# Kernel optimization log

Hardware: AMD Instinct MI355X
Metric: run time of the kernel (lower is better)

## Reference

```python
import jax, jax.numpy as jnp
import numpy as np

B, T, N, C = 4, 6, 512, 8
HID, FEAT, EMB, IN_DIM = 64, 16, 32, 1
KS, KC, HORIZON = 3, 2, 3
ALPHA = 3.0

def _init(key, shape):
    fin = shape[-2] if len(shape) >= 2 else shape[-1]
    return jax.random.normal(key, shape, dtype=jnp.float32) * (1.0 / fin) ** 0.5

def setup_inputs():
    ks = jax.random.split(jax.random.key(0), 32)
    L_enc = (IN_DIM + FEAT + HID) * KS * KC
    L_dec = (HID + FEAT + HID) * KS * KC
    return {
        "X_seq": jax.random.normal(ks[0], (B, T, N, C), dtype=jnp.float32),
        "As": jax.random.uniform(ks[1], (N, N), dtype=jnp.float32) / N,
        "Ac": jax.random.uniform(ks[2], (C, C), dtype=jnp.float32) / C,
        "feature": jax.random.normal(ks[3], (N, FEAT), dtype=jnp.float32),
        "Wu_S": _init(ks[4], (C, HID)), "Wv_S": _init(ks[5], (C, HID)),
        "Wu_C": _init(ks[6], (N, HID)), "Wv_C": _init(ks[7], (N, HID)),
        "mfS_w1": _init(ks[8], (4, 2, 256)), "mfS_b1": jnp.zeros((4, 256), jnp.float32),
        "mfS_w2": _init(ks[9], (4, 256, 256)), "mfS_b2": jnp.zeros((4, 256), jnp.float32),
        "mfC_w1": _init(ks[10], (4, 2, 256)), "mfC_b1": jnp.zeros((4, 256), jnp.float32),
        "mfC_w2": _init(ks[11], (4, 256, 256)), "mfC_b2": jnp.zeros((4, 256), jnp.float32),
        "enc_gW": _init(ks[12], (L_enc, 2 * HID)), "enc_gb": jnp.zeros((2 * HID,), jnp.float32),
        "enc_cW": _init(ks[13], (L_enc, HID)), "enc_cb": jnp.zeros((HID,), jnp.float32),
        "dec_gW": _init(ks[14], (L_dec, 2 * HID)), "dec_gb": jnp.zeros((2 * HID,), jnp.float32),
        "dec_cW": _init(ks[15], (L_dec, HID)), "dec_cb": jnp.zeros((HID,), jnp.float32),
        "out_w1": _init(ks[16], (HID, EMB)), "out_b1": jnp.zeros((EMB,), jnp.float32),
        "out_w2": _init(ks[17], (EMB, IN_DIM)), "out_b2": jnp.zeros((IN_DIM,), jnp.float32),
    }

def _mlp(x, w1, b1, w2, b2):
    return jax.nn.relu(x @ w1 + b1) @ w2 + b2

def _mixed_fusion(A, P, w1, b1, w2, b2):
    # node_feat = [rowsum(A), rowsum(P)]; key/value MLPs indexed 0:key_A 1:key_P 2:val_A 3:val_P
    nf = jnp.stack([A.sum(-1), P.sum(-1)], axis=-1)            # [n, 2]
    An, Pn = A @ nf, P @ nf
    key = _mlp(An, w1[0], b1[0], w2[0], b2[0]) + _mlp(Pn, w1[1], b1[1], w2[1], b2[1])
    val = _mlp(An, w1[2], b1[2], w2[2], b2[2]) + _mlp(Pn, w1[3], b1[3], w2[3], b2[3])
    a = jax.nn.sigmoid(key @ val.T)
    return a * A + (1.0 - a) * P

def _adaptive_graph(Xf, Wu, Wv):
    U = jnp.tanh(ALPHA * Xf @ Wu)                              # [b,t,n,h]
    V = jnp.tanh(ALPHA * Xf @ Wv)
    M = jnp.einsum('btnh,btmh->nm', U, V)
    # Ps = softmax(relu(M - M^T)) matches einsum pair in torch source
    return jax.nn.softmax(jax.nn.relu(M - M.T), axis=-1)

def _cheby(G, K):
    mats = [jnp.eye(G.shape[0], dtype=G.dtype), G]
    for _ in range(2, K):
        mats.append(2.0 * G @ mats[-1] - mats[-2])
    return jnp.stack(mats[:K], axis=0)                         # [K, n, n]

def _bdg(X, Gs_set, Gc_set, W, b):
    # X: [b,n,c,l]; fused Ks x Kc Chebyshev mode products; cat order (k, j, l) matches torch cat
    t1 = jnp.einsum('bncl,knm->kbmcl', X, Gs_set)
    t2 = jnp.einsum('kbmcl,jcd->bmdkjl', t1, Gc_set)
    feat = t2.reshape(t2.shape[0], t2.shape[1], t2.shape[2], -1)
    return feat @ W + b

def _cell(Xt, Ht, featx, Gs_set, Gc_set, gW, gb, cW, cb):
    XH = jnp.concatenate([Xt, Ht, featx], axis=-1)
    uv = _bdg(XH, Gs_set, Gc_set, gW, gb)
    update = jax.nn.sigmoid(uv[..., :HID])
    reset = jax.nn.sigmoid(uv[..., HID:])
    cand_in = jnp.concatenate([Xt, reset * Ht, featx], axis=-1)
    cand = jnp.tanh(_bdg(cand_in, Gs_set, Gc_set, cW, cb))
    return (1.0 - update) * Ht + update * cand

def _forward(X_seq, As, Ac, feature, Wu_S, Wv_S, Wu_C, Wv_C,
             mfS_w1, mfS_b1, mfS_w2, mfS_b2, mfC_w1, mfC_b1, mfC_w2, mfC_b2,
             enc_gW, enc_gb, enc_cW, enc_cb, dec_gW, dec_gb, dec_cW, dec_cb,
             out_w1, out_b1, out_w2, out_b2):
    # MGP_Gen: adaptive spatial / categorical graphs fused with priors
    Ps = _adaptive_graph(X_seq, Wu_S, Wv_S)
    Gs = _mixed_fusion(As, Ps, mfS_w1, mfS_b1, mfS_w2, mfS_b2)
    Xc = jnp.swapaxes(X_seq, 2, 3)                             # [b,t,c,n]
    Pc = _adaptive_graph(Xc, Wu_C, Wv_C)
    Gc = _mixed_fusion(Ac, Pc, mfC_w1, mfC_b1, mfC_w2, mfC_b2)
    Gs_set, Gc_set = _cheby(Gs, KS), _cheby(Gc, KC)
    featx = jnp.broadcast_to(feature[None, :, None, :], (B, N, C, FEAT))
    X5 = X_seq[..., None]                                      # [b,t,n,c,1]
    Ht = jnp.zeros((B, N, C, HID), dtype=X_seq.dtype)
    for t in range(T):                                         # encoder GRU over history
        Ht = _cell(X5[:, t], Ht, featx, Gs_set, Gc_set, enc_gW, enc_gb, enc_cW, enc_cb)
    deco_in, Hd = Ht, Ht
    outs = []
    for _ in range(HORIZON):
        Hd = _cell(deco_in, Hd, featx, Gs_set, Gc_set, dec_gW, dec_gb, dec_cW, dec_cb)
        outs.append(_mlp(Hd, out_w1, out_b1, out_w2, out_b2))
        deco_in = Hd
    return jnp.stack(outs, axis=1)                             # [b, horizon, n, c, 1]

def reference(X_seq, As, Ac, feature, Wu_S, Wv_S, Wu_C, Wv_C, mfS_w1, mfS_b1, mfS_w2, mfS_b2, mfC_w1, mfC_b1, mfC_w2, mfC_b2, enc_gW, enc_gb, enc_cW, enc_cb, dec_gW, dec_gb, dec_cW, dec_cb, out_w1, out_b1, out_w2, out_b2):
    return _forward(X_seq, As, Ac, feature, Wu_S, Wv_S, Wu_C, Wv_C, mfS_w1, mfS_b1, mfS_w2, mfS_b2, mfC_w1, mfC_b1, mfC_w2, mfC_b2, enc_gW, enc_gb, enc_cW, enc_cb, dec_gW, dec_gb, dec_cW, dec_cb, out_w1, out_b1, out_w2, out_b2)
```

## Files before the change

### kernel.cpp

```cpp
#include <hip/hip_runtime.h>
#include <math.h>

constexpr int kB = 4, kT = 6, kN = 512, kC = 8;
constexpr int kH = 64, kF = 16, kE = 32;
constexpr int kKS = 3, kKC = 2, kHOR = 3;
constexpr int kBT = kB * kT;
constexpr int kRK = kBT * kH;
constexpr int L_ENC = 1 + kH + kF;
constexpr int L_DEC = kH + kH + kF;
constexpr int PL_ENC = 96;
constexpr int PL_DEC = 160;
constexpr int KP_ENC = 3 * PL_ENC;
constexpr int KP_DEC = 3 * PL_DEC;
constexpr float kALPHA = 3.0f;

typedef unsigned short ushortT;
typedef short short8 __attribute__((ext_vector_type(8)));
typedef float f32x4 __attribute__((ext_vector_type(4)));

__device__ __forceinline__ float sigm(float x) { return 1.0f / (1.0f + __expf(-x)); }

__device__ __forceinline__ ushortT f2bf(float f) {
    union { float f; unsigned int u; } v; v.f = f;
    unsigned int r = v.u + 0x7fffu + ((v.u >> 16) & 1u);
    return (ushortT)(r >> 16);
}

__device__ __forceinline__ void fma44(const float4& a, const float4& b, float acc[4][4]) {
    acc[0][0] += a.x*b.x; acc[0][1] += a.x*b.y; acc[0][2] += a.x*b.z; acc[0][3] += a.x*b.w;
    acc[1][0] += a.y*b.x; acc[1][1] += a.y*b.y; acc[1][2] += a.y*b.z; acc[1][3] += a.y*b.w;
    acc[2][0] += a.z*b.x; acc[2][1] += a.z*b.y; acc[2][2] += a.z*b.z; acc[2][3] += a.z*b.w;
    acc[3][0] += a.w*b.x; acc[3][1] += a.w*b.y; acc[3][2] += a.w*b.z; acc[3][3] += a.w*b.w;
}


__global__ __launch_bounds__(256) void k_uvproj_s(
    const float* __restrict__ X, const float* __restrict__ Wu, const float* __restrict__ Wv,
    float* __restrict__ Upr, float* __restrict__ Vpr)
{
    int idx = blockIdx.x * blockDim.x + threadIdx.x;
    if (idx >= kN * kBT * kH) return;
    int h = idx % kH; int bt = (idx / kH) % kBT; int n = idx / (kH * kBT);
    const float* xr = X + ((size_t)bt * kN + n) * kC;
    float u = 0.f, v = 0.f;
#pragma unroll
    for (int c = 0; c < kC; ++c) { float x = xr[c]; u += x * Wu[c*kH + h]; v += x * Wv[c*kH + h]; }
    Upr[(size_t)n * kRK + bt * kH + h] = tanhf(kALPHA * u);
    Vpr[(size_t)n * kRK + bt * kH + h] = tanhf(kALPHA * v);
}

__global__ __launch_bounds__(512) void k_uvproj_c2(
    const float* __restrict__ X, const float* __restrict__ WuC, const float* __restrict__ WvC,
    float* __restrict__ Uc, float* __restrict__ Vc)
{
    __shared__ float Xs[4096];
    __shared__ float Wus[4096], Wvs[4096];
    int bt = blockIdx.x, tid = threadIdx.x;
    for (int i = tid; i < 4096; i += 512) Xs[i] = X[(size_t)bt*4096 + i];
    int c = tid >> 6, h = tid & 63;
    float u = 0.f, v = 0.f;
    for (int n0 = 0; n0 < 512; n0 += 64) {
        __syncthreads();
        for (int i = tid; i < 4096; i += 512) { Wus[i] = WuC[n0*64 + i]; Wvs[i] = WvC[n0*64 + i]; }
        __syncthreads();
#pragma unroll 8
        for (int nn = 0; nn < 64; ++nn) {
            float x = Xs[(n0+nn)*8 + c];
            u += x * Wus[nn*64 + h];
            v += x * Wvs[nn*64 + h];
        }
    }
    Uc[(size_t)bt*512 + c*64 + h] = tanhf(kALPHA * u);
    Vc[(size_t)bt*512 + c*64 + h] = tanhf(kALPHA * v);
}

__global__ __launch_bounds__(512) void k_mc2(
    const float* __restrict__ Uc, const float* __restrict__ Vc, float* __restrict__ Mc)
{
    __shared__ float red[512];
    int tid = threadIdx.x;
    int cd = tid & 63, kc = tid >> 6;
    int c = cd >> 3, d = cd & 7;
    float s = 0.f;
    for (int q = kc*192; q < kc*192 + 192; ++q) {
        int bt = q >> 6, h = q & 63;
        s += Uc[(size_t)bt*512 + c*64 + h] * Vc[(size_t)bt*512 + d*64 + h];
    }
    red[tid] = s; __syncthreads();
    for (int st = 256; st >= 64; st >>= 1) { if (tid < st) red[tid] += red[tid + st]; __syncthreads(); }
    if (tid < 64) Mc[tid] = red[tid];
}

__global__ __launch_bounds__(256) void k_nfa(const float* __restrict__ A, float* __restrict__ nf)
{
    int i = blockIdx.x, tid = threadIdx.x;
// ... 147 lines not shown
        rsA[i] = a;
    }
    __syncthreads();
    if (tid < 16) {
        int i = tid >> 1, comp = tid & 1;
        float an = 0.f, pn = 0.f;
#pragma unroll
        for (int j = 0; j < 8; ++j) {
            float nfj = comp ? 1.f : rsA[j];
            an += Ac[i*8+j] * nfj; pn += Pcs[i*8+j] * nfj;
        }
        Ans[i*2+comp] = an; Pns[i*2+comp] = pn;
    }
    __syncthreads();
    for (int e = tid; e < 2048; e += 256) {
        int i = e >> 8, o = e & 255;
        hA[i][o] = fmaxf(Ans[i*2]*w1[qa*512 + o] + Ans[i*2+1]*w1[qa*512 + 256 + o] + b1[qa*256 + o], 0.f);
        hP[i][o] = fmaxf(Pns[i*2]*w1[qp*512 + o] + Pns[i*2+1]*w1[qp*512 + 256 + o] + b1[qp*256 + o], 0.f);
    }
    __syncthreads();
    for (int e = tid; e < 512; e += 256) {
        int i = e >> 6, oc = c0 + (e & 63);
        float s = b2[qa*256 + oc] + b2[qp*256 + oc];
        for (int k = 0; k < 256; ++k)
            s += hA[i][k]*w2[(size_t)qa*65536 + k*256 + oc] + hP[i][k]*w2[(size_t)qp*65536 + k*256 + oc];
        keyval[(size_t)kv*2048 + i*256 + oc] = s;
    }
}

__global__ void k_gcfuse2(const float* __restrict__ keyval, const float* __restrict__ Mc,
                          const float* __restrict__ Ac, float* __restrict__ GcF)
{
    __shared__ float Pcs[64];
    int t = threadIdx.x; if (t >= 64) return;
    if (t < 8) {
        int i = t;
        float row[8]; float mx = -1e30f;
#pragma unroll
        for (int j = 0; j < 8; ++j) { float v = fmaxf(Mc[i*8+j] - Mc[j*8+i], 0.f); row[j] = v; mx = fmaxf(mx, v); }
        float s = 0.f;
#pragma unroll
        for (int j = 0; j < 8; ++j) { row[j] = __expf(row[j] - mx); s += row[j]; }
        float inv = 1.f / s;
#pragma unroll
        for (int j = 0; j < 8; ++j) Pcs[i*8+j] = row[j] * inv;
    }
    __syncthreads();
    int c = t >> 3, d = t & 7;
    const float* key = keyval;
    const float* val = keyval + 2048;
    float s = 0.f;
    for (int k = 0; k < 256; ++k) s += key[c*256 + k] * val[d*256 + k];
    float a = sigm(s);
    GcF[c*8 + d] = a*Ac[c*8 + d] + (1.f - a)*Pcs[c*8 + d];
}


__global__ void k_transp(const float* __restrict__ G, ushortT* __restrict__ Gt)
{
    __shared__ float tile[32][33];
    int bx = blockIdx.x * 32, by = blockIdx.y * 32;
    int x = threadIdx.x, y0 = threadIdx.y;
    for (int yy = y0; yy < 32; yy += 8) tile[yy][x] = G[(size_t)(by+yy)*kN + bx + x];
    __syncthreads();
    for (int yy = y0; yy < 32; yy += 8) Gt[(size_t)(bx+yy)*kN + by + x] = f2bf(tile[x][yy]);
}

__global__ __launch_bounds__(256) void k_prep_wt(
    const float* __restrict__ W, ushortT* __restrict__ WT,
    int L, int PL, int KP, int outW, int mode)
{
    int idx = blockIdx.x * blockDim.x + threadIdx.x;
    if (idx >= 2 * outW * KP) return;
    int qp = idx % KP, o = idx / KP;
    int kk = qp / PL, l = qp - kk * PL;
    int lo;
    if (mode == 1) lo = (l < 64) ? l + 1 : (l == 64) ? 0 : (l < 80) ? L : (l - 15);
    else lo = l;
    int j = o / outW, oo = o - j * outW;
    float v = (lo < L) ? W[(size_t)((kk*2 + j)*L + lo) * outW + oo] : 0.f;
    WT[idx] = f2bf(v);
}

__global__ __launch_bounds__(256) void k_cheby_mfma(
    const ushortT* __restrict__ Gst, ushortT* __restrict__ Gst2)
{
    __shared__ short sA[128][40];
    __shared__ short sB[128][40];
    int tid = threadIdx.x;
    int m0 = blockIdx.y * 128, j0 = blockIdx.x * 128;
    int w = tid >> 6, lane = tid & 63, wr = w >> 1, wc = w & 1;
    f32x4 acc[4][4];
#pragma unroll
    for (int i = 0; i < 4; ++i)
#pragma unroll
        for (int j = 0; j < 4; ++j) acc[i][j] = (f32x4){0.f, 0.f, 0.f, 0.f};
    for (int k0 = 0; k0 < kN; k0 += 32) {
        {
            int row = tid >> 1, lc = (tid & 1) * 16;
            const ushortT* p = Gst + (size_t)(m0 + row)*kN + k0 + lc;
            *(short8*)&sA[row][lc]     = *(const short8*)p;
            *(short8*)&sA[row][lc + 8] = *(const short8*)(p + 8);
        }
        {
            int kr = tid & 31, jc = (tid >> 5) * 8;
#pragma unroll
            for (int rep = 0; rep < 2; ++rep) {
                short8 v = *(const short8*)(Gst + (size_t)(k0 + kr)*kN + j0 + jc + rep*64);
#pragma unroll
                for (int i = 0; i < 8; ++i) sB[jc + rep*64 + i][kr] = v[i];
            }
        }
        __syncthreads();
        short8 af[4], bfr[4];
#pragma unroll
        for (int mi = 0; mi < 4; ++mi)
            af[mi] = *(const short8*)&sA[wr*64 + mi*16 + (lane & 15)][(lane >> 4) * 8];
#pragma unroll
        for (int ni = 0; ni < 4; ++ni)
            bfr[ni] = *(const short8*)&sB[wc*64 + ni*16 + (lane & 15)][(lane >> 4) * 8];
#pragma unroll
        for (int mi = 0; mi < 4; ++mi)
#pragma unroll
            for (int ni = 0; ni < 4; ++ni)
                acc[mi][ni] = __builtin_amdgcn_mfma_f32_16x16x32_bf16(af[mi], bfr[ni], acc[mi][ni], 0, 0, 0);
        __syncthreads();
    }
#pragma unroll
    for (int mi = 0; mi < 4; ++mi) {
#pragma unroll
        for (int ni = 0; ni < 4; ++ni) {
            int row0 = m0 + wr*64 + mi*16 + (lane >> 4) * 4;
            int col  = j0 + wc*64 + ni*16 + (lane & 15);
#pragma unroll
            for (int q = 0; q < 4; ++q) {
                int row = row0 + q;
                Gst2[(size_t)row*kN + col] = f2bf(2.f*acc[mi][ni][q] - (row == col ? 1.f : 0.f));
            }
        }
    }
}

template<int CLP, int PL, int ACTW, int OFF>
__global__ __launch_bounds__(256) void k_t1m(
    const ushortT* __restrict__ Gst, const ushortT* __restrict__ Xin, ushortT* __restrict__ Yout)
{
    __shared__ short sA[128][40];
    __shared__ short sB[128][40];
    int tid = threadIdx.x;
    int ki = blockIdx.z >> 2, b = blockIdx.z & 3;
    const ushortT* A = Gst + (size_t)ki * kN * kN;
    const ushortT* B = Xin + (size_t)b * kN * CLP;
    ushortT* C = Yout + (size_t)(ki*4 + b) * kN * CLP;
    int m0 = blockIdx.y * 128, j0 = blockIdx.x * 128;
    int w = tid >> 6, lane = tid & 63, wr = w >> 1, wc = w & 1;
    f32x4 acc[4][4];
#pragma unroll
    for (int i = 0; i < 4; ++i)
#pragma unroll
        for (int j = 0; j < 4; ++j) acc[i][j] = (f32x4){0.f, 0.f, 0.f, 0.f};

    for (int k0 = 0; k0 < kN; k0 += 32) {
        {
            int row = tid >> 1, lc = (tid & 1) * 16;
            const ushortT* p = A + (size_t)(m0 + row)*kN + k0 + lc;
            *(short8*)&sA[row][lc]     = *(const short8*)p;
            *(short8*)&sA[row][lc + 8] = *(const short8*)(p + 8);
        }
        {
            int kr = tid & 31, jc = (tid >> 5) * 8;
#pragma unroll
            for (int rep = 0; rep < 2; ++rep) {
                int j = j0 + jc + rep*64;
                int cg = j / ACTW;
                int col = cg*PL + OFF + (j - cg*ACTW);
                short8 v = *(const short8*)(B + (size_t)(k0 + kr)*CLP + col);
#pragma unroll
                for (int i = 0; i < 8; ++i) sB[jc + rep*64 + i][kr] = v[i];
            }
        }
        __syncthreads();
        short8 af[4], bfr[4];
#pragma unroll
        for (int mi = 0; mi < 4; ++mi)
            af[mi] = *(const short8*)&sA[wr*64 + mi*16 + (lane & 15)][(lane >> 4) * 8];
#pragma unroll
        for (int ni = 0; ni < 4; ++ni)
            bfr[ni] = *(const short8*)&sB[wc*64 + ni*16 + (lane & 15)][(lane >> 4) * 8];
#pragma unroll
        for (int mi = 0; mi < 4; ++mi)
#pragma unroll
            for (int ni = 0; ni < 4; ++ni)
                acc[mi][ni] = __builtin_amdgcn_mfma_f32_16x16x32_bf16(af[mi], bfr[ni], acc[mi][ni], 0, 0, 0);
        __syncthreads();
    }
#pragma unroll
    for (int mi = 0; mi < 4; ++mi) {
#pragma unroll
        for (int ni = 0; ni < 4; ++ni) {
            int row = m0 + wr*64 + mi*16 + (lane >> 4) * 4;
            int fj = j0 + wc*64 + ni*16;
            int cg = fj / ACTW;
            int col = cg*PL + OFF + (fj - cg*ACTW) + (lane & 15);
#pragma unroll
            for (int q = 0; q < 4; ++q)
                C[(size_t)(row + q)*CLP + col] = f2bf(acc[mi][ni][q]);
        }
    }
}

template<int PL, int KP, int XOFF>
__global__ __launch_bounds__(256) void k_gates_f(
    ushortT* __restrict__ XH, const ushortT* __restrict__ Yb,
    const ushortT* __restrict__ WT, const float* __restrict__ GcM,
    const float* __restrict__ gb, const float* __restrict__ Ht,
    float* __restrict__ upd)
{
    __shared__ short sA[64][40];
    __shared__ short sB[256][40];
    __shared__ float sEp[32][260];
    __shared__ float GcS[64], gbS[128];
    int tid = threadIdx.x;
    int r0 = blockIdx.x * 64;
    int b = r0 >> 12, rr = r0 & 4095;
    const ushortT* src0 = XH + (size_t)r0 * PL;
    const ushortT* src1 = Yb + ((size_t)b * 4096 + rr) * PL;
    const ushortT* src2 = Yb + ((size_t)(4 + b) * 4096 + rr) * PL;
    if (tid < 64) GcS[tid] = GcM[tid];
    if (tid >= 64 && tid < 192) gbS[tid - 64] = gb[tid - 64];
    int w = tid >> 6, lane = tid & 63;
    f32x4 acc[4][4];
#pragma unroll
    for (int i = 0; i < 4; ++i)
#pragma unroll
        for (int j = 0; j < 4; ++j) acc[i][j] = (f32x4){0.f, 0.f, 0.f, 0.f};

    for (int k0 = 0; k0 < KP; k0 += 32) {
        int kk = k0 / PL, l0 = k0 - kk * PL;
        const ushortT* Ap = (kk == 0) ? src0 : (kk == 1) ? src1 : src2;
        {
            int row = tid >> 2, lc = (tid & 3) * 8;
            *(short8*)&sA[row][lc] = *(const short8*)(Ap + (size_t)row*PL + l0 + lc);
        }
        {
            const ushortT* p = WT + (size_t)tid*KP + k0;
            *(short8*)&sB[tid][0]  = *(const short8*)(p);
            *(short8*)&sB[tid][8]  = *(const short8*)(p + 8);
            *(short8*)&sB[tid][16] = *(const short8*)(p + 16);
            *(short8*)&sB[tid][24] = *(const short8*)(p + 24);
        }
        __syncthreads();
        short8 af[4], bfr[4];
#pragma unroll
        for (int mi = 0; mi < 4; ++mi)
            af[mi] = *(const short8*)&sA[mi*16 + (lane & 15)][(lane >> 4) * 8];
#pragma unroll
        for (int ni = 0; ni < 4; ++ni)
            bfr[ni] = *(const short8*)&sB[w*64 + ni*16 + (lane & 15)][(lane >> 4) * 8];
#pragma unroll
        for (int mi = 0; mi < 4; ++mi)
#pragma unroll
            for (int ni = 0; ni < 4; ++ni)
                acc[mi][ni] = __builtin_amdgcn_mfma_f32_16x16x32_bf16(af[mi], bfr[ni], acc[mi][ni], 0, 0, 0);
        __syncthreads();
    }
    for (int chunk = 0; chunk < 2; ++chunk) {
#pragma unroll
        for (int mi2 = 0; mi2 < 2; ++mi2) {
            int mi = chunk*2 + mi2;
#pragma unroll
            for (int ni = 0; ni < 4; ++ni)
#pragma unroll
                for (int q = 0; q < 4; ++q)
                    sEp[mi2*16 + (lane >> 4)*4 + q][w*64 + ni*16 + (lane & 15)] = acc[mi][ni][q];
        }
        __syncthreads();
        for (int it = 0; it < 16; ++it) {
            int idx = it*256 + tid;
            int o = idx & 127, rloc = idx >> 7;
            int r = r0 + chunk*32 + rloc;
            int d = r & 7, bb = rloc & ~7;
            float pre = sEp[rloc][o] + gbS[o];
#pragma unroll
            for (int c = 0; c < 8; ++c) pre += GcS[c*8 + d] * sEp[bb + c][128 + o];
            float g = sigm(pre);
            if (o < 64) upd[(size_t)r*64 + o] = g;
            else {
                int h = o - 64;
                XH[(size_t)r*PL + XOFF + h] = f2bf(g * Ht[(size_t)r*64 + h]);
            }
        }
        __syncthreads();
    }
}

template<int PL, int KP>
__global__ __launch_bounds__(256) void k_cand_f(
    const ushortT* __restrict__ XH, const ushortT* __restrict__ Yb,
    const ushortT* __restrict__ WT, const float* __restrict__ GcM,
    const float* __restrict__ cb, const float* __restrict__ upd,
    float* __restrict__ Ht)
{
    __shared__ short sA[64][40];
    __shared__ short sB[128][40];
    __shared__ float sEp[64][132];
    __shared__ float GcS[64], cbS[64];
    int tid = threadIdx.x;
    int r0 = blockIdx.x * 64;
    int b = r0 >> 12, rr = r0 & 4095;
    const ushortT* src0 = XH + (size_t)r0 * PL;
    const ushortT* src1 = Yb + ((size_t)b * 4096 + rr) * PL;
    const ushortT* src2 = Yb + ((size_t)(4 + b) * 4096 + rr) * PL;
    if (tid < 64) GcS[tid] = GcM[tid];
    if (tid >= 64 && tid < 128) cbS[tid - 64] = cb[tid - 64];
    int w = tid >> 6, lane = tid & 63;
    f32x4 acc[4][2];
#pragma unroll
    for (int i = 0; i < 4; ++i)
#pragma unroll
        for (int j = 0; j < 2; ++j) acc[i][j] = (f32x4){0.f, 0.f, 0.f, 0.f};

    for (int k0 = 0; k0 < KP; k0 += 32) {
        int kk = k0 / PL, l0 = k0 - kk * PL;
        const ushortT* Ap = (kk == 0) ? src0 : (kk == 1) ? src1 : src2;
        {
            int row = tid >> 2, lc = (tid & 3) * 8;
            *(short8*)&sA[row][lc] = *(const short8*)(Ap + (size_t)row*PL + l0 + lc);
        }
        {
            int col = tid >> 1, seg = (tid & 1) * 16;
            const ushortT* p = WT + (size_t)col*KP + k0 + seg;
            *(short8*)&sB[col][seg]     = *(const short8*)p;
            *(short8*)&sB[col][seg + 8] = *(const short8*)(p + 8);
        }
        __syncthreads();
        short8 af[4], bfr[2];
#pragma unroll
        for (int mi = 0; mi < 4; ++mi)
            af[mi] = *(const short8*)&sA[mi*16 + (lane & 15)][(lane >> 4) * 8];
#pragma unroll
        for (int ni = 0; ni < 2; ++ni)
            bfr[ni] = *(const short8*)&sB[w*32 + ni*16 + (lane & 15)][(lane >> 4) * 8];
#pragma unroll
        for (int mi = 0; mi < 4; ++mi)
#pragma unroll
            for (int ni = 0; ni < 2; ++ni)
                acc[mi][ni] = __builtin_amdgcn_mfma_f32_16x16x32_bf16(af[mi], bfr[ni], acc[mi][ni], 0, 0, 0);
        __syncthreads();
    }
#pragma unroll
    for (int mi = 0; mi < 4; ++mi)
#pragma unroll
        for (int ni = 0; ni < 2; ++ni)
#pragma unroll
            for (int q = 0; q < 4; ++q)
                sEp[mi*16 + (lane >> 4)*4 + q][w*32 + ni*16 + (lane & 15)] = acc[mi][ni][q];
    __syncthreads();
    for (int it = 0; it < 16; ++it) {
        int idx = it*256 + tid;
        int o = idx & 63, rloc = idx >> 6;
        int r = r0 + rloc;
        int d = r & 7, bb = rloc & ~7;
        float pre = sEp[rloc][o] + cbS[o];
#pragma unroll
        for (int c = 0; c < 8; ++c) pre += GcS[c*8 + d] * sEp[bb + c][64 + o];
        float cv = tanhf(pre);
        float u = upd[(size_t)r*64 + o];
        float h0 = Ht[(size_t)r*64 + o];
        Ht[(size_t)r*64 + o] = (1.f - u)*h0 + u*cv;
    }
}


__global__ __launch_bounds__(256) void k_build_enc(
    const float* __restrict__ X, int t, const float* __restrict__ Ht,
    const float* __restrict__ featr, ushortT* __restrict__ XH)
{
    int idx = blockIdx.x * blockDim.x + threadIdx.x;
    if (idx >= 16384 * PL_ENC) return;
    int l = idx % PL_ENC; int r = idx / PL_ENC;
    int c = r & 7; int m = (r >> 3) & 511; int b = r >> 12;
    float v;
    if (l < 64)            v = Ht[(size_t)r*kH + l];
    else if (l == 64)      v = X[(((size_t)b*kT + t)*kN + m)*kC + c];
    else if (l < 80)       v = 0.f;
    else                   v = featr[m*kF + (l - 80)];
    XH[idx] = f2bf(v);
}

__global__ __launch_bounds__(256) void k_build_dec(
    const float* __restrict__ Ht, const float* __restrict__ featr, ushortT* __restrict__ XH)
{
    int idx = blockIdx.x * blockDim.x + threadIdx.x;
    if (idx >= 16384 * PL_DEC) return;
    int l = idx % PL_DEC; int r = idx / PL_DEC;
    int m = (r >> 3) & 511;
    float v;
    if (l < kH)            v = Ht[(size_t)r*kH + l];
    else if (l < 2*kH)     v = Ht[(size_t)r*kH + l - kH];
    else if (l < L_DEC)    v = featr[m*kF + l - 2*kH];
    else                   v = 0.f;
    XH[idx] = f2bf(v);
}

__global__ __launch_bounds__(256) void k_outmlp(
    const float* __restrict__ Hd, const float* __restrict__ w1, const float* __restrict__ b1,
    const float* __restrict__ w2, const float* __restrict__ b2, float* __restrict__ out, int hz)
{
    int idx = blockIdx.x * blockDim.x + threadIdx.x;
    if (idx >= kB*kN*kC) return;
    int c = idx % kC; int m = (idx / kC) % kN; int b = idx / (kC*kN);
    const float* h = Hd + (size_t)idx * kH;
    float hreg[kH];
#pragma unroll
    for (int k = 0; k < kH; ++k) hreg[k] = h[k];
    float acc = b2[0];
    for (int e = 0; e < kE; ++e) {
        float s = b1[e];
#pragma unroll
        for (int k = 0; k < kH; ++k) s += hreg[k] * w1[k*kE + e];
        acc += fmaxf(s, 0.f) * w2[e];
    }
    out[((size_t)(b*kHOR + hz)*kN + m)*kC + c] = acc;
}

extern "C" void kernel_launch(void* const* d_in, const int* in_sizes, int n_in,
                              void* d_out, int out_size, void* d_ws, size_t ws_size,
                              hipStream_t stream)
{
    (void)in_sizes; (void)n_in; (void)out_size; (void)ws_size;
    const float* X      = (const float*)d_in[0];
    const float* As     = (const float*)d_in[1];
    const float* Ac     = (const float*)d_in[2];
    const float* featr  = (const float*)d_in[3];
    const float* WuS    = (const float*)d_in[4];
    const float* WvS    = (const float*)d_in[5];
    const float* WuC    = (const float*)d_in[6];
    const float* WvC    = (const float*)d_in[7];
    const float* mfS_w1 = (const float*)d_in[8];
    const float* mfS_b1 = (const float*)d_in[9];
    const float* mfS_w2 = (const float*)d_in[10];
    const float* mfS_b2 = (const float*)d_in[11];
    const float* mfC_w1 = (const float*)d_in[12];
    const float* mfC_b1 = (const float*)d_in[13];
    const float* mfC_w2 = (const float*)d_in[14];
    const float* mfC_b2 = (const float*)d_in[15];
    const float* enc_gW = (const float*)d_in[16];
    const float* enc_gb = (const float*)d_in[17];
    const float* enc_cW = (const float*)d_in[18];
    const float* enc_cb = (const float*)d_in[19];
    const float* dec_gW = (const float*)d_in[20];
    const float* dec_gb = (const float*)d_in[21];
    const float* dec_cW = (const float*)d_in[22];
    const float* dec_cb = (const float*)d_in[23];
    const float* out_w1 = (const float*)d_in[24];
    const float* out_b1 = (const float*)d_in[25];
    const float* out_w2 = (const float*)d_in[26];
    const float* out_b2 = (const float*)d_in[27];
    float* out = (float*)d_out;
    float* ws = (float*)d_ws;

    float* Ht     = ws;
    float* updb   = Ht + 1048576;
    float* Gg     = updb + 1048576;
    float* Gs     = Gg + 4194304;
    float* smallf = Gs + 262144;
    float* nfS = smallf;
    float* AnS = nfS + 1024;
    float* PnS = AnS + 1024;
    float* McB = PnS + 1024;
    float* GcF = McB + 64;
    float* kvC = GcF + 64;
    ushortT* XHb  = (ushortT*)(smallf + 8192);
    ushortT* Yb   = XHb + 2621440;
    ushortT* GstB = Yb + 5242880;
    ushortT* WTg_e = GstB + 524288;
    ushortT* WTc_e = WTg_e + 73728;
    ushortT* WTg_d = WTc_e + 36864;
    ushortT* WTc_d = WTg_d + 122880;
    float* Upr   = Gg;
    float* Vpr   = Upr + 786432;
    float* part  = Vpr + 786432;
    float* Ms    = part + 1048576;
    float* Ps    = Ms + 262144;
    float* hidAP = Ps + 262144;
    float* keyS  = hidAP + 262144;
    float* valS  = keyS + 131072;
    float* w2tK  = valS + 131072;
    float* w2tV  = w2tK + 131072;
    float* Uc    = w2tV + 131072;
    float* Vc    = Uc + 12288;

    constexpr int CLP_ENC = kC * PL_ENC;
    constexpr int CLP_DEC = kC * PL_DEC;

    hipMemsetAsync(Ht, 0, (size_t)16384 * kH * sizeof(float), stream);

    k_prep_wt<<<(2*128*KP_ENC + 255)/256, 256, 0, stream>>>(enc_gW, WTg_e, L_ENC, PL_ENC, KP_ENC, 128, 1);
    k_prep_wt<<<(2*64 *KP_ENC + 255)/256, 256, 0, stream>>>(enc_cW, WTc_e, L_ENC, PL_ENC, KP_ENC, 64, 1);
    k_prep_wt<<<(2*128*KP_DEC + 255)/256, 256, 0, stream>>>(dec_gW, WTg_d, L_DEC, PL_DEC, KP_DEC, 128, 0);
    k_prep_wt<<<(2*64 *KP_DEC + 255)/256, 256, 0, stream>>>(dec_cW, WTc_d, L_DEC, PL_DEC, KP_DEC, 64, 0);
    k_prep_w2t<<<512, 256, 0, stream>>>(mfS_w2, w2tK, w2tV);

    k_uvproj_s<<<(kN*kBT*kH + 255)/256, 256, 0, stream>>>(X, WuS, WvS, Upr, Vpr);
    k_gemm_ntsk<<<dim3(8, 8, 4), 256, 0, stream>>>(Upr, Vpr, part, 512, 512, 1536, 384);
    k_redep<<<1024, 256, 0, stream>>>(part, 4, 262144, 512, Ms, 0, nullptr, nullptr);
    k_nfa<<<kN, 256, 0, stream>>>(As, nfS);
    k_softmax_anpn<<<kN, 256, 0, stream>>>(Ms, As, nfS, Ps, AnS, PnS);
    k_mlp1cat<<<1024, 256, 0, stream>>>(AnS, PnS, mfS_w1, mfS_b1, 0, 1, hidAP);
    k_gemm_ntsk<<<dim3(4, 8, 2), 256, 0, stream>>>(hidAP, w2tK, part, 512, 256, 512, 256);
    k_redep<<<512, 256, 0, stream>>>(part, 2, 131072, 256, keyS, 2, mfS_b2, mfS_b2 + 256);
    k_mlp1cat<<<1024, 256, 0, stream>>>(AnS, PnS, mfS_w1, mfS_b1, 2, 3, hidAP);
    k_gemm_ntsk<<<dim3(4, 8, 2), 256, 0, stream>>>(hidAP, w2tV, part, 512, 256, 512, 256);
    k_redep<<<512, 256, 0, stream>>>(part, 2, 131072, 256, valS, 2, mfS_b2 + 512, mfS_b2 + 768);
    k_gemm_ntsk<<<dim3(8, 8, 2), 256, 0, stream>>>(keyS, valS, part, 512, 512, 256, 128);
    k_redep<<<1024, 256, 0, stream>>>(part, 2, 262144, 512, Gs, 1, As, Ps);
    k_transp<<<dim3(16, 16), dim3(32, 8), 0, stream>>>(Gs, GstB);
    k_cheby_mfma<<<dim3(4, 4), 256, 0, stream>>>(GstB, GstB + 262144);

    k_uvproj_c2<<<kBT, 512, 0, stream>>>(X, WuC, WvC, Uc, Vc);
    k_mc2<<<1, 512, 0, stream>>>(Uc, Vc, McB);
    k_catmlp2<<<dim3(2, 4), 256, 0, stream>>>(McB, Ac, mfC_w1, mfC_b1, mfC_w2, mfC_b2, kvC);
    k_gcfuse2<<<1, 64, 0, stream>>>(kvC, McB, Ac, GcF);

    bool featDone = false;
    for (int t = 0; t < kT; ++t) {
        k_build_enc<<<(16384*PL_ENC + 255)/256, 256, 0, stream>>>(X, t, Ht, featr, XHb);
        if (!featDone) {
            k_t1m<CLP_ENC, PL_ENC, 16, 80><<<dim3(1, 4, 8), 256, 0, stream>>>(GstB, XHb, Yb);
            featDone = true;
        }
        k_t1m<CLP_ENC, PL_ENC, 80, 0><<<dim3(5, 4, 8), 256, 0, stream>>>(GstB, XHb, Yb);
        k_gates_f<PL_ENC, KP_ENC, 0><<<256, 256, 0, stream>>>(XHb, Yb, WTg_e, GcF, enc_gb, Ht, updb);
        k_t1m<CLP_ENC, PL_ENC, 64, 0><<<dim3(4, 4, 8), 256, 0, stream>>>(GstB, XHb, Yb);
        k_cand_f<PL_ENC, KP_ENC><<<256, 256, 0, stream>>>(XHb, Yb, WTc_e, GcF, enc_cb, updb, Ht);
    }

    featDone = false;
    for (int hz = 0; hz < kHOR; ++hz) {
        k_build_dec<<<(16384*PL_DEC + 255)/256, 256, 0, stream>>>(Ht, featr, XHb);
        if (!featDone) {
            k_t1m<CLP_DEC, PL_DEC, 16, 128><<<dim3(1, 4, 8), 256, 0, stream>>>(GstB, XHb, Yb);
            featDone = true;
        }
        k_t1m<CLP_DEC, PL_DEC, 128, 0><<<dim3(8, 4, 8), 256, 0, stream>>>(GstB, XHb, Yb);
        k_gates_f<PL_DEC, KP_DEC, 64><<<256, 256, 0, stream>>>(XHb, Yb, WTg_d, GcF, dec_gb, Ht, updb);
        k_t1m<CLP_DEC, PL_DEC, 64, 64><<<dim3(4, 4, 8), 256, 0, stream>>>(GstB, XHb, Yb);
        k_cand_f<PL_DEC, KP_DEC><<<256, 256, 0, stream>>>(XHb, Yb, WTc_d, GcF, dec_cb, updb, Ht);
        k_outmlp<<<(kB*kN*kC + 255)/256, 256, 0, stream>>>(Ht, out_w1, out_b1, out_w2, out_b2, out, hz);
    }
}
```

Measured before the change: 1.078 ms.

## Split gate GEMMs from epilogues, fold decoder duplicate input weights, fuse state builds

Each fused gate and candidate kernel becomes two kernels. The first is a 128-row MFMA GEMM that writes fp32 pre-activations to a scratch buffer, and the second is a per-node epilogue that applies the Gc channel mix and the nonlinearity. The decoder gate weights for the duplicated hidden input are pre-summed so K shrinks from 480 to 288, and its graph propagation only handles 64 columns instead of 128. The per-step build_enc/build_dec kernels are removed by having the candidate epilogue write the next bf16 input row, including the next X value. The output MLP is fused into the decoder epilogue. In exchange, fp32 intermediates make an extra round-trip through global memory.

```diff
diff --git a/kernel.cpp b/kernel.cpp
--- a/kernel.cpp
+++ b/kernel.cpp
@@ -11,6 +11,7 @@
 constexpr int PL_ENC = 96;
 constexpr int PL_DEC = 160;
 constexpr int KP_ENC = 3 * PL_ENC;
+constexpr int KP_DGF = 288;
 constexpr int KP_DEC = 3 * PL_DEC;
 constexpr float kALPHA = 3.0f;
 
@@ -324,6 +325,22 @@
     WT[idx] = f2bf(v);
 }
 
+__global__ __launch_bounds__(256) void k_prep_wtgd(
+    const float* __restrict__ W, ushortT* __restrict__ WT)
+{
+    int idx = blockIdx.x * blockDim.x + threadIdx.x;
+    if (idx >= 256 * KP_DGF) return;
+    int qp = idx % KP_DGF, o = idx / KP_DGF;
+    int k = qp / 96, p = qp - k * 96;
+    int j = o >> 7, oo = o & 127;
+    int base = (k*2 + j) * L_DEC;
+    float v;
+    if (p < 64)      v = W[(size_t)(base + p)*128 + oo] + W[(size_t)(base + 64 + p)*128 + oo];
+    else if (p < 80) v = W[(size_t)(base + 128 + (p - 64))*128 + oo];
+    else             v = 0.f;
+    WT[idx] = f2bf(v);
+}
+
 __global__ __launch_bounds__(256) void k_cheby_mfma(
     const ushortT* __restrict__ Gst, ushortT* __restrict__ Gst2)
 {
@@ -396,6 +413,10 @@
     ushortT* C = Yout + (size_t)(ki*4 + b) * kN * CLP;
     int m0 = blockIdx.y * 128, j0 = blockIdx.x * 128;
     int w = tid >> 6, lane = tid & 63, wr = w >> 1, wc = w & 1;
+    int kr = tid & 31, jc = (tid >> 5) * 8;
+    int colr0, colr1;
+    { int j = j0 + jc;      int cg = j / ACTW; colr0 = cg*PL + OFF + (j - cg*ACTW); }
+    { int j = j0 + jc + 64; int cg = j / ACTW; colr1 = cg*PL + OFF + (j - cg*ACTW); }
     f32x4 acc[4][4];
 #pragma unroll
     for (int i = 0; i < 4; ++i)
@@ -410,16 +431,12 @@
             *(short8*)&sA[row][lc + 8] = *(const short8*)(p + 8);
         }
         {
-            int kr = tid & 31, jc = (tid >> 5) * 8;
-#pragma unroll
-            for (int rep = 0; rep < 2; ++rep) {
-                int j = j0 + jc + rep*64;
-                int cg = j / ACTW;
-                int col = cg*PL + OFF + (j - cg*ACTW);
-                short8 v = *(const short8*)(B + (size_t)(k0 + kr)*CLP + col);
-#pragma unroll
-                for (int i = 0; i < 8; ++i) sB[jc + rep*64 + i][kr] = v[i];
-            }
+            short8 v0 = *(const short8*)(B + (size_t)(k0 + kr)*CLP + colr0);
+            short8 v1 = *(const short8*)(B + (size_t)(k0 + kr)*CLP + colr1);
+#pragma unroll
+            for (int i = 0; i < 8; ++i) sB[jc + i][kr] = v0[i];
+#pragma unroll
+            for (int i = 0; i < 8; ++i) sB[jc + 64 + i][kr] = v1[i];
         }
         __syncthreads();
         short8 af[4], bfr[4];
@@ -451,219 +468,193 @@
     }
 }
 
-template<int PL, int KP, int XOFF>
-__global__ __launch_bounds__(256) void k_gates_f(
-    ushortT* __restrict__ XH, const ushortT* __restrict__ Yb,
-    const ushortT* __restrict__ WT, const float* __restrict__ GcM,
-    const float* __restrict__ gb, const float* __restrict__ Ht,
-    float* __restrict__ upd)
-{
-    __shared__ short sA[64][40];
-    __shared__ short sB[256][40];
-    __shared__ float sEp[32][260];
-    __shared__ float GcS[64], gbS[128];
+template<int PL, int NQ, int MODE, int FN>
+__global__ __launch_bounds__(256) void k_gg(
+    const ushortT* __restrict__ XH, const ushortT* __restrict__ Yb,
+    const ushortT* __restrict__ WT, float* __restrict__ Cout)
+{
+    constexpr int BN = 32 * FN;
+    constexpr int KP = NQ * 32;
+    constexpr int Ntot = 64 * FN;
+    __shared__ short sA[128][40];
+    __shared__ short sB[BN][40];
     int tid = threadIdx.x;
-    int r0 = blockIdx.x * 64;
+    int r0 = blockIdx.y * 128, j0 = blockIdx.x * BN;
     int b = r0 >> 12, rr = r0 & 4095;
     const ushortT* src0 = XH + (size_t)r0 * PL;
-    const ushortT* src1 = Yb + ((size_t)b * 4096 + rr) * PL;
+    const ushortT* src1 = Yb + ((size_t)b       * 4096 + rr) * PL;
     const ushortT* src2 = Yb + ((size_t)(4 + b) * 4096 + rr) * PL;
-    if (tid < 64) GcS[tid] = GcM[tid];
-    if (tid >= 64 && tid < 192) gbS[tid - 64] = gb[tid - 64];
-    int w = tid >> 6, lane = tid & 63;
-    f32x4 acc[4][4];
+    int w = tid >> 6, lane = tid & 63, wr = w >> 1, wc = w & 1;
+    f32x4 acc[4][FN];
 #pragma unroll
     for (int i = 0; i < 4; ++i)
 #pragma unroll
-        for (int j = 0; j < 4; ++j) acc[i][j] = (f32x4){0.f, 0.f, 0.f, 0.f};
-
-    for (int k0 = 0; k0 < KP; k0 += 32) {
-        int kk = k0 / PL, l0 = k0 - kk * PL;
-        const ushortT* Ap = (kk == 0) ? src0 : (kk == 1) ? src1 : src2;
+        for (int j = 0; j < FN; ++j) acc[i][j] = (f32x4){0.f, 0.f, 0.f, 0.f};
+
+    for (int q = 0; q < NQ; ++q) {
+        int k, off;
+        if (MODE == 0)      { k = q/3; off = (q - k*3)*32; }
+        else if (MODE == 1) { k = q/3; int part = q - k*3; off = (part < 2) ? part*32 : 128; }
+        else                { k = q/5; off = (q - k*5)*32; }
+        const ushortT* Ap = (k == 0) ? src0 : (k == 1) ? src1 : src2;
         {
-            int row = tid >> 2, lc = (tid & 3) * 8;
-            *(short8*)&sA[row][lc] = *(const short8*)(Ap + (size_t)row*PL + l0 + lc);
-        }
-        {
-            const ushortT* p = WT + (size_t)tid*KP + k0;
-            *(short8*)&sB[tid][0]  = *(const short8*)(p);
-            *(short8*)&sB[tid][8]  = *(const short8*)(p + 8);
-            *(short8*)&sB[tid][16] = *(const short8*)(p + 16);
-            *(short8*)&sB[tid][24] = *(const short8*)(p + 24);
-        }
-        __syncthreads();
-        short8 af[4], bfr[4];
-#pragma unroll
-        for (int mi = 0; mi < 4; ++mi)
-            af[mi] = *(const short8*)&sA[mi*16 + (lane & 15)][(lane >> 4) * 8];
-#pragma unroll
-        for (int ni = 0; ni < 4; ++ni)
-            bfr[ni] = *(const short8*)&sB[w*64 + ni*16 + (lane & 15)][(lane >> 4) * 8];
-#pragma unroll
-        for (int mi = 0; mi < 4; ++mi)
-#pragma unroll
-            for (int ni = 0; ni < 4; ++ni)
-                acc[mi][ni] = __builtin_amdgcn_mfma_f32_16x16x32_bf16(af[mi], bfr[ni], acc[mi][ni], 0, 0, 0);
-        __syncthreads();
-    }
-    for (int chunk = 0; chunk < 2; ++chunk) {
-#pragma unroll
-        for (int mi2 = 0; mi2 < 2; ++mi2) {
-            int mi = chunk*2 + mi2;
-#pragma unroll
-            for (int ni = 0; ni < 4; ++ni)
-#pragma unroll
-                for (int q = 0; q < 4; ++q)
-                    sEp[mi2*16 + (lane >> 4)*4 + q][w*64 + ni*16 + (lane & 15)] = acc[mi][ni][q];
-        }
-        __syncthreads();
-        for (int it = 0; it < 16; ++it) {
-            int idx = it*256 + tid;
-            int o = idx & 127, rloc = idx >> 7;
-            int r = r0 + chunk*32 + rloc;
-            int d = r & 7, bb = rloc & ~7;
-            float pre = sEp[rloc][o] + gbS[o];
-#pragma unroll
-            for (int c = 0; c < 8; ++c) pre += GcS[c*8 + d] * sEp[bb + c][128 + o];
-            float g = sigm(pre);
-            if (o < 64) upd[(size_t)r*64 + o] = g;
-            else {
-                int h = o - 64;
-                XH[(size_t)r*PL + XOFF + h] = f2bf(g * Ht[(size_t)r*64 + h]);
-            }
-        }
-        __syncthreads();
-    }
-}
-
-template<int PL, int KP>
-__global__ __launch_bounds__(256) void k_cand_f(
-    const ushortT* __restrict__ XH, const ushortT* __restrict__ Yb,
-    const ushortT* __restrict__ WT, const float* __restrict__ GcM,
-    const float* __restrict__ cb, const float* __restrict__ upd,
-    float* __restrict__ Ht)
-{
-    __shared__ short sA[64][40];
-    __shared__ short sB[128][40];
-    __shared__ float sEp[64][132];
-    __shared__ float GcS[64], cbS[64];
-    int tid = threadIdx.x;
-    int r0 = blockIdx.x * 64;
-    int b = r0 >> 12, rr = r0 & 4095;
-    const ushortT* src0 = XH + (size_t)r0 * PL;
-    const ushortT* src1 = Yb + ((size_t)b * 4096 + rr) * PL;
-    const ushortT* src2 = Yb + ((size_t)(4 + b) * 4096 + rr) * PL;
-    if (tid < 64) GcS[tid] = GcM[tid];
-    if (tid >= 64 && tid < 128) cbS[tid - 64] = cb[tid - 64];
-    int w = tid >> 6, lane = tid & 63;
-    f32x4 acc[4][2];
-#pragma unroll
-    for (int i = 0; i < 4; ++i)
-#pragma unroll
-        for (int j = 0; j < 2; ++j) acc[i][j] = (f32x4){0.f, 0.f, 0.f, 0.f};
-
-    for (int k0 = 0; k0 < KP; k0 += 32) {
-        int kk = k0 / PL, l0 = k0 - kk * PL;
-        const ushortT* Ap = (kk == 0) ? src0 : (kk == 1) ? src1 : src2;
-        {
-            int row = tid >> 2, lc = (tid & 3) * 8;
-            *(short8*)&sA[row][lc] = *(const short8*)(Ap + (size_t)row*PL + l0 + lc);
-        }
-        {
+            int row = tid >> 1, lc = (tid & 1) * 16;
+            const ushortT* p = Ap + (size_t)row * PL + off + lc;
+            *(short8*)&sA[row][lc]     = *(const short8*)p;
+            *(short8*)&sA[row][lc + 8] = *(const short8*)(p + 8);
+        }
+        if (FN == 4) {
             int col = tid >> 1, seg = (tid & 1) * 16;
-            const ushortT* p = WT + (size_t)col*KP + k0 + seg;
+            const ushortT* p = WT + (size_t)(j0 + col)*KP + q*32 + seg;
             *(short8*)&sB[col][seg]     = *(const short8*)p;
             *(short8*)&sB[col][seg + 8] = *(const short8*)(p + 8);
-        }
-        __syncthreads();
-        short8 af[4], bfr[2];
+        } else {
+            int col = tid >> 2, seg = (tid & 3) * 8;
+            *(short8*)&sB[col][seg] = *(const short8*)(WT + (size_t)(j0 + col)*KP + q*32 + seg);
+        }
+        __syncthreads();
+        short8 af[4], bfr[FN];
 #pragma unroll
         for (int mi = 0; mi < 4; ++mi)
-            af[mi] = *(const short8*)&sA[mi*16 + (lane & 15)][(lane >> 4) * 8];
-#pragma unroll
-        for (int ni = 0; ni < 2; ++ni)
-            bfr[ni] = *(const short8*)&sB[w*32 + ni*16 + (lane & 15)][(lane >> 4) * 8];
+            af[mi] = *(const short8*)&sA[wr*64 + mi*16 + (lane & 15)][(lane >> 4) * 8];
+#pragma unroll
+        for (int ni = 0; ni < FN; ++ni)
+            bfr[ni] = *(const short8*)&sB[wc*16*FN + ni*16 + (lane & 15)][(lane >> 4) * 8];
 #pragma unroll
         for (int mi = 0; mi < 4; ++mi)
 #pragma unroll
-            for (int ni = 0; ni < 2; ++ni)
+            for (int ni = 0; ni < FN; ++ni)
                 acc[mi][ni] = __builtin_amdgcn_mfma_f32_16x16x32_bf16(af[mi], bfr[ni], acc[mi][ni], 0, 0, 0);
         __syncthreads();
     }
 #pragma unroll
-    for (int mi = 0; mi < 4; ++mi)
-#pragma unroll
-        for (int ni = 0; ni < 2; ++ni)
+    for (int mi = 0; mi < 4; ++mi) {
+#pragma unroll
+        for (int ni = 0; ni < FN; ++ni) {
+            int row = r0 + wr*64 + mi*16 + (lane >> 4) * 4;
+            int col = j0 + wc*16*FN + ni*16 + (lane & 15);
 #pragma unroll
             for (int q = 0; q < 4; ++q)
-                sEp[mi*16 + (lane >> 4)*4 + q][w*32 + ni*16 + (lane & 15)] = acc[mi][ni][q];
+                Cout[(size_t)(row + q)*Ntot + col] = acc[mi][ni][q];
+        }
+    }
+}
+
+
+template<int PL, int XOFF>
+__global__ __launch_bounds__(256) void k_gates_ep(
+    const float* __restrict__ Gg, const float* __restrict__ GcM,
+    const float* __restrict__ gb, const float* __restrict__ Ht,
+    float* __restrict__ upd, ushortT* __restrict__ XH)
+{
+    __shared__ float sG[8][256];
+    __shared__ float GcS[64];
+    int tid = threadIdx.x, bm = blockIdx.x;
+    const float* src = Gg + (size_t)bm * 2048;
+    for (int i = tid; i < 2048; i += 256) sG[i >> 8][i & 255] = src[i];
+    if (tid < 64) GcS[tid] = GcM[tid];
     __syncthreads();
-    for (int it = 0; it < 16; ++it) {
-        int idx = it*256 + tid;
-        int o = idx & 63, rloc = idx >> 6;
-        int r = r0 + rloc;
-        int d = r & 7, bb = rloc & ~7;
-        float pre = sEp[rloc][o] + cbS[o];
-#pragma unroll
-        for (int c = 0; c < 8; ++c) pre += GcS[c*8 + d] * sEp[bb + c][64 + o];
+    int d = tid >> 5, o0 = (tid & 31) * 4;
+    size_t rb = (size_t)bm * 8 + d;
+#pragma unroll
+    for (int q = 0; q < 4; ++q) {
+        int o = o0 + q;
+        float pre = sG[d][o] + gb[o];
+#pragma unroll
+        for (int c = 0; c < 8; ++c) pre += GcS[c*8 + d] * sG[c][128 + o];
+        float g = sigm(pre);
+        if (o < kH) upd[rb*kH + o] = g;
+        else {
+            int h = o - kH;
+            XH[rb*PL + XOFF + h] = f2bf(g * Ht[rb*kH + h]);
+        }
+    }
+}
+
+template<int MODE>
+__global__ __launch_bounds__(256) void k_cand_ep(
+    const float* __restrict__ Gc2, const float* __restrict__ GcM,
+    const float* __restrict__ cb, const float* __restrict__ upd,
+    float* __restrict__ Ht, ushortT* __restrict__ XHo,
+    const float* __restrict__ X, int tnext,
+    const float* __restrict__ ow1, const float* __restrict__ ob1,
+    const float* __restrict__ ow2, const float* __restrict__ ob2,
+    float* __restrict__ out, int hz)
+{
+    __shared__ float sG[8][128];
+    __shared__ float GcS[64];
+    __shared__ float Hn[8][65];
+    __shared__ float Pp[8][32];
+    int tid = threadIdx.x, bm = blockIdx.x;
+    const float* src = Gc2 + (size_t)bm * 1024;
+    for (int i = tid; i < 1024; i += 256) sG[i >> 7][i & 127] = src[i];
+    if (tid < 64) GcS[tid] = GcM[tid];
+    __syncthreads();
+    int d = tid >> 5, o0 = (tid & 31) * 2;
+    size_t rb = (size_t)bm * 8 + d;
+#pragma unroll
+    for (int jj = 0; jj < 2; ++jj) {
+        int o = o0 + jj;
+        float pre = sG[d][o] + cb[o];
+#pragma unroll
+        for (int c = 0; c < 8; ++c) pre += GcS[c*8 + d] * sG[c][64 + o];
         float cv = tanhf(pre);
-        float u = upd[(size_t)r*64 + o];
-        float h0 = Ht[(size_t)r*64 + o];
-        Ht[(size_t)r*64 + o] = (1.f - u)*h0 + u*cv;
-    }
-}
-
-
-__global__ __launch_bounds__(256) void k_build_enc(
-    const float* __restrict__ X, int t, const float* __restrict__ Ht,
-    const float* __restrict__ featr, ushortT* __restrict__ XH)
+        float u = upd[rb*kH + o];
+        float h0 = Ht[rb*kH + o];
+        float hn = (1.f - u)*h0 + u*cv;
+        Ht[rb*kH + o] = hn;
+        if (MODE >= 2) Hn[d][o] = hn;
+        if (MODE == 0)      XHo[rb*PL_ENC + o] = f2bf(hn);
+        else if (MODE <= 2) XHo[rb*PL_DEC + o] = f2bf(hn);
+    }
+    if (MODE == 0) {
+        if (tid < 8) {
+            int r = bm*8 + tid;
+            int c2 = r & 7, m = (r >> 3) & 511, b2 = r >> 12;
+            XHo[(size_t)r*PL_ENC + 64] = f2bf(X[(((size_t)b2*kT + tnext)*kN + m)*kC + c2]);
+        }
+    }
+    if (MODE >= 2) {
+        __syncthreads();
+        int row = tid >> 5, e = tid & 31;
+        float s = ob1[e];
+#pragma unroll
+        for (int k = 0; k < kH; ++k) s += Hn[row][k] * ow1[k*kE + e];
+        Pp[row][e] = fmaxf(s, 0.f) * ow2[e];
+        __syncthreads();
+        if (tid < 8) {
+            float v = ob2[0];
+#pragma unroll
+            for (int e2 = 0; e2 < 32; ++e2) v += Pp[tid][e2];
+            int r = bm*8 + tid;
+            int c2 = r & 7, m = (r >> 3) & 511, b2 = r >> 12;
+            out[((size_t)(b2*kHOR + hz)*kN + m)*kC + c2] = v;
+        }
+    }
+}
+
+__global__ __launch_bounds__(256) void k_build_enc0(
+    const float* __restrict__ X, const float* __restrict__ featr, ushortT* __restrict__ XH)
 {
     int idx = blockIdx.x * blockDim.x + threadIdx.x;
     if (idx >= 16384 * PL_ENC) return;
     int l = idx % PL_ENC; int r = idx / PL_ENC;
-    int c = r & 7; int m = (r >> 3) & 511; int b = r >> 12;
     float v;
-    if (l < 64)            v = Ht[(size_t)r*kH + l];
-    else if (l == 64)      v = X[(((size_t)b*kT + t)*kN + m)*kC + c];
-    else if (l < 80)       v = 0.f;
-    else                   v = featr[m*kF + (l - 80)];
+    if (l < 64)       v = 0.f;
+    else if (l == 64) { int c = r & 7, m = (r >> 3) & 511, b = r >> 12; v = X[(((size_t)b*kT)*kN + m)*kC + c]; }
+    else if (l < 80)  v = 0.f;
+    else              { int m = (r >> 3) & 511; v = featr[m*kF + (l - 80)]; }
     XH[idx] = f2bf(v);
 }
 
-__global__ __launch_bounds__(256) void k_build_dec(
-    const float* __restrict__ Ht, const float* __restrict__ featr, ushortT* __restrict__ XH)
+__global__ __launch_bounds__(256) void k_initdec(
+    const float* __restrict__ featr, ushortT* __restrict__ XHd)
 {
     int idx = blockIdx.x * blockDim.x + threadIdx.x;
-    if (idx >= 16384 * PL_DEC) return;
-    int l = idx % PL_DEC; int r = idx / PL_DEC;
-    int m = (r >> 3) & 511;
-    float v;
-    if (l < kH)            v = Ht[(size_t)r*kH + l];
-    else if (l < 2*kH)     v = Ht[(size_t)r*kH + l - kH];
-    else if (l < L_DEC)    v = featr[m*kF + l - 2*kH];
-    else                   v = 0.f;
-    XH[idx] = f2bf(v);
-}
-
-__global__ __launch_bounds__(256) void k_outmlp(
-    const float* __restrict__ Hd, const float* __restrict__ w1, const float* __restrict__ b1,
-    const float* __restrict__ w2, const float* __restrict__ b2, float* __restrict__ out, int hz)
-{
-    int idx = blockIdx.x * blockDim.x + threadIdx.x;
-    if (idx >= kB*kN*kC) return;
-    int c = idx % kC; int m = (idx / kC) % kN; int b = idx / (kC*kN);
-    const float* h = Hd + (size_t)idx * kH;
-    float hreg[kH];
-#pragma unroll
-    for (int k = 0; k < kH; ++k) hreg[k] = h[k];
-    float acc = b2[0];
-    for (int e = 0; e < kE; ++e) {
-        float s = b1[e];
-#pragma unroll
-        for (int k = 0; k < kH; ++k) s += hreg[k] * w1[k*kE + e];
-        acc += fmaxf(s, 0.f) * w2[e];
-    }
-    out[((size_t)(b*kHOR + hz)*kN + m)*kC + c] = acc;
+    if (idx >= 16384 * 32) return;
+    int l2 = idx & 31; int r = idx >> 5;
+    float v = (l2 < 16) ? featr[((r >> 3) & 511)*kF + l2] : 0.f;
+    XHd[(size_t)r*PL_DEC + 128 + l2] = f2bf(v);
 }
 
 extern "C" void kernel_launch(void* const* d_in, const int* in_sizes, int n_in,
@@ -720,6 +711,7 @@
     ushortT* WTc_e = WTg_e + 73728;
     ushortT* WTg_d = WTc_e + 36864;
     ushortT* WTc_d = WTg_d + 122880;
+    ushortT* XHd   = WTc_d + 61440;
     float* Upr   = Gg;
     float* Vpr   = Upr + 786432;
     float* part  = Vpr + 786432;
@@ -740,7 +732,7 @@
 
     k_prep_wt<<<(2*128*KP_ENC + 255)/256, 256, 0, stream>>>(enc_gW, WTg_e, L_ENC, PL_ENC, KP_ENC, 128, 1);
     k_prep_wt<<<(2*64 *KP_ENC + 255)/256, 256, 0, stream>>>(enc_cW, WTc_e, L_ENC, PL_ENC, KP_ENC, 64, 1);
-    k_prep_wt<<<(2*128*KP_DEC + 255)/256, 256, 0, stream>>>(dec_gW, WTg_d, L_DEC, PL_DEC, KP_DEC, 128, 0);
+    k_prep_wtgd<<<(256*KP_DGF + 255)/256, 256, 0, stream>>>(dec_gW, WTg_d);
     k_prep_wt<<<(2*64 *KP_DEC + 255)/256, 256, 0, stream>>>(dec_cW, WTc_d, L_DEC, PL_DEC, KP_DEC, 64, 0);
     k_prep_w2t<<<512, 256, 0, stream>>>(mfS_w2, w2tK, w2tV);
 
@@ -765,30 +757,36 @@
     k_catmlp2<<<dim3(2, 4), 256, 0, stream>>>(McB, Ac, mfC_w1, mfC_b1, mfC_w2, mfC_b2, kvC);
     k_gcfuse2<<<1, 64, 0, stream>>>(kvC, McB, Ac, GcF);
 
-    bool featDone = false;
+    k_build_enc0<<<(16384*PL_ENC + 255)/256, 256, 0, stream>>>(X, featr, XHb);
+    k_initdec<<<(16384*32 + 255)/256, 256, 0, stream>>>(featr, XHd);
+
+    k_t1m<CLP_ENC, PL_ENC, 16, 80><<<dim3(1, 4, 8), 256, 0, stream>>>(GstB, XHb, Yb);
     for (int t = 0; t < kT; ++t) {
-        k_build_enc<<<(16384*PL_ENC + 255)/256, 256, 0, stream>>>(X, t, Ht, featr, XHb);
-        if (!featDone) {
-            k_t1m<CLP_ENC, PL_ENC, 16, 80><<<dim3(1, 4, 8), 256, 0, stream>>>(GstB, XHb, Yb);
-            featDone = true;
-        }
         k_t1m<CLP_ENC, PL_ENC, 80, 0><<<dim3(5, 4, 8), 256, 0, stream>>>(GstB, XHb, Yb);
-        k_gates_f<PL_ENC, KP_ENC, 0><<<256, 256, 0, stream>>>(XHb, Yb, WTg_e, GcF, enc_gb, Ht, updb);
+        k_gg<PL_ENC, 9, 0, 4><<<dim3(2, 128), 256, 0, stream>>>(XHb, Yb, WTg_e, Gg);
+        k_gates_ep<PL_ENC, 0><<<2048, 256, 0, stream>>>(Gg, GcF, enc_gb, Ht, updb, XHb);
         k_t1m<CLP_ENC, PL_ENC, 64, 0><<<dim3(4, 4, 8), 256, 0, stream>>>(GstB, XHb, Yb);
-        k_cand_f<PL_ENC, KP_ENC><<<256, 256, 0, stream>>>(XHb, Yb, WTc_e, GcF, enc_cb, updb, Ht);
-    }
-
-    featDone = false;
+        k_gg<PL_ENC, 9, 0, 2><<<dim3(2, 128), 256, 0, stream>>>(XHb, Yb, WTc_e, Gg);
+        if (t < kT - 1)
+            k_cand_ep<0><<<2048, 256, 0, stream>>>(Gg, GcF, enc_cb, updb, Ht, XHb, X, t + 1,
+                                                   nullptr, nullptr, nullptr, nullptr, nullptr, 0);
+        else
+            k_cand_ep<1><<<2048, 256, 0, stream>>>(Gg, GcF, enc_cb, updb, Ht, XHd, nullptr, 0,
+                                                   nullptr, nullptr, nullptr, nullptr, nullptr, 0);
+    }
+
+    k_t1m<CLP_DEC, PL_DEC, 16, 128><<<dim3(1, 4, 8), 256, 0, stream>>>(GstB, XHd, Yb);
     for (int hz = 0; hz < kHOR; ++hz) {
-        k_build_dec<<<(16384*PL_DEC + 255)/256, 256, 0, stream>>>(Ht, featr, XHb);
-        if (!featDone) {
-            k_t1m<CLP_DEC, PL_DEC, 16, 128><<<dim3(1, 4, 8), 256, 0, stream>>>(GstB, XHb, Yb);
-            featDone = true;
-        }
-        k_t1m<CLP_DEC, PL_DEC, 128, 0><<<dim3(8, 4, 8), 256, 0, stream>>>(GstB, XHb, Yb);
-        k_gates_f<PL_DEC, KP_DEC, 64><<<256, 256, 0, stream>>>(XHb, Yb, WTg_d, GcF, dec_gb, Ht, updb);
-        k_t1m<CLP_DEC, PL_DEC, 64, 64><<<dim3(4, 4, 8), 256, 0, stream>>>(GstB, XHb, Yb);
-        k_cand_f<PL_DEC, KP_DEC><<<256, 256, 0, stream>>>(XHb, Yb, WTc_d, GcF, dec_cb, updb, Ht);
-        k_outmlp<<<(kB*kN*kC + 255)/256, 256, 0, stream>>>(Ht, out_w1, out_b1, out_w2, out_b2, out, hz);
-    }
-}
+        k_t1m<CLP_DEC, PL_DEC, 64, 0><<<dim3(4, 4, 8), 256, 0, stream>>>(GstB, XHd, Yb);
+        k_gg<PL_DEC, 9, 1, 4><<<dim3(2, 128), 256, 0, stream>>>(XHd, Yb, WTg_d, Gg);
+        k_gates_ep<PL_DEC, 64><<<2048, 256, 0, stream>>>(Gg, GcF, dec_gb, Ht, updb, XHd);
+        k_t1m<CLP_DEC, PL_DEC, 64, 64><<<dim3(4, 4, 8), 256, 0, stream>>>(GstB, XHd, Yb);
+        k_gg<PL_DEC, 15, 2, 2><<<dim3(2, 128), 256, 0, stream>>>(XHd, Yb, WTc_d, Gg);
+        if (hz < kHOR - 1)
+            k_cand_ep<2><<<2048, 256, 0, stream>>>(Gg, GcF, dec_cb, updb, Ht, XHd, nullptr, 0,
+                                                   out_w1, out_b1, out_w2, out_b2, out, hz);
+        else
+            k_cand_ep<3><<<2048, 256, 0, stream>>>(Gg, GcF, dec_cb, updb, Ht, XHd, nullptr, 0,
+                                                   out_w1, out_b1, out_w2, out_b2, out, hz);
+    }
+}
```

Result: faster. 973.1 us (-9.7%).
